# Kernel optimization log

Hardware: AMD Instinct MI355X
Metric: run time of the kernel (lower is better)

Reference implementation:

```python
import jax, jax.numpy as jnp
import numpy as np

SCALING = 2.0  # lora_alpha / r


def setup_inputs() -> dict:
    key = jax.random.key(0)
    ks = jax.random.split(key, 6)
    B, S, D_IN, D_OUT, R = 4, 4096, 4096, 4096, 32
    x = jax.random.normal(ks[0], (B, S, D_IN), dtype=jnp.float32)
    W = jax.random.normal(ks[1], (D_OUT, D_IN), dtype=jnp.float32) * 0.02
    b = jax.random.normal(ks[2], (D_OUT,), dtype=jnp.float32) * 0.02
    A = jax.random.normal(ks[3], (R, D_IN), dtype=jnp.float32) * 0.02
    B_w = jax.random.normal(ks[4], (D_OUT, R), dtype=jnp.float32) * 0.02
    # per-sample activation offsets, in [1, S]
    alora_offsets = jax.random.randint(ks[5], (B,), 1, S + 1, dtype=jnp.int32)
    return {"x": x, "alora_offsets": alora_offsets, "W": W, "b": b, "A": A, "B_w": B_w}


def reference(x, alora_offsets, W, b, A, B_w):
    # base linear: y = x @ W^T + b
    base = jnp.einsum("bsd,od->bso", x, W) + b  # [B, S, D_OUT]
    # LoRA path on full sequence (dropout is identity at inference, p=0)
    lora = jnp.einsum("bsr,or->bso", jnp.einsum("bsd,rd->bsr", x, A), B_w) * SCALING
    # per-sample tail mask: only last k = min(offset, S) positions get the LoRA update
    S = x.shape[1]
    k = jnp.minimum(alora_offsets, S)  # [B]
    pos = jnp.arange(S, dtype=jnp.int32)
    mask = pos[None, :] >= (S - k)[:, None]  # [B, S] True on the tail
    return base + jnp.where(mask[:, :, None], lora, jnp.zeros((), base.dtype))
```

## Files before the change

kernel.cpp:

```cpp
#include <hip/hip_runtime.h>
#include <hip/hip_bf16.h>

typedef __attribute__((ext_vector_type(8))) short short8;
typedef __attribute__((ext_vector_type(4))) float f32x4;

#define GLOAD_LDS16(gp, lp)                                                      \
  __builtin_amdgcn_global_load_lds(                                              \
      (const __attribute__((address_space(1))) void*)(gp),                       \
      (__attribute__((address_space(3))) void*)(lp), 16, 0, 0)

#define SBAR() asm volatile("s_barrier" ::: "memory")
#define VMC(n)                                                                   \
  do {                                                                           \
    asm volatile("s_waitcnt vmcnt(" #n ")" ::: "memory");                        \
    __builtin_amdgcn_sched_barrier(0);                                           \
  } while (0)

__device__ __forceinline__ unsigned short f2bf_rne(float f) {
  union { float f; unsigned int u; } v; v.f = f;
  unsigned int u = v.u;
  u += 0x7fffu + ((u >> 16) & 1u);
  return (unsigned short)(u >> 16);
}

__device__ __forceinline__ short8 pack8(f32x4 a, f32x4 b) {
  short8 o;
  o[0] = (short)f2bf_rne(a[0]); o[1] = (short)f2bf_rne(a[1]);
  o[2] = (short)f2bf_rne(a[2]); o[3] = (short)f2bf_rne(a[3]);
  o[4] = (short)f2bf_rne(b[0]); o[5] = (short)f2bf_rne(b[1]);
  o[6] = (short)f2bf_rne(b[2]); o[7] = (short)f2bf_rne(b[3]);
  return o;
}

__global__ __launch_bounds__(256) void cvt_lora_kernel(
    const float* __restrict__ x,
    const float* __restrict__ A,
    const float* __restrict__ W,
    const float* __restrict__ Bw,
    const int* __restrict__ offs,
    unsigned short* __restrict__ xb,
    unsigned short* __restrict__ Wb,
    unsigned short* __restrict__ Bwb,
    unsigned short* __restrict__ T)
{
  __shared__ unsigned short xs[32 * 72];
  __shared__ unsigned short as_[32 * 72];
  const int t = threadIdx.x;
  const int m0 = blockIdx.x * 32;
  const int l = t & 63, w = t >> 6;
  const int wr = w >> 1, wc = w & 1;
  const int lr = l & 15, lk = (l >> 4) * 8;
  const int arow = t >> 3, acol = (t & 7) * 8;

  if (blockIdx.x < 64) {
    int idx = blockIdx.x * 256 + t;
    const f32x4* s4b = (const f32x4*)Bw;
    ((short8*)Bwb)[idx] = pack8(s4b[2 * idx], s4b[2 * idx + 1]);
  }

  const float* px = x + (size_t)(m0 + arow) * 4096 + acol;
  const float* pa = A + (size_t)arow * 4096 + acol;
  f32x4 vx0 = *(const f32x4*)px, vx1 = *(const f32x4*)(px + 4);
  f32x4 va0 = *(const f32x4*)pa, va1 = *(const f32x4*)(pa + 4);

  f32x4 acc = {0, 0, 0, 0};
  for (int kt = 0; kt < 64; ++kt) {
    short8 s0 = pack8(vx0, vx1);
    short8 sa = pack8(va0, va1);
    if (kt < 63) {
      px += 64; pa += 64;
      vx0 = *(const f32x4*)px; vx1 = *(const f32x4*)(px + 4);
      va0 = *(const f32x4*)pa; va1 = *(const f32x4*)(pa + 4);
    }
    *(short8*)(xb + (size_t)(m0 + arow) * 4096 + kt * 64 + acol) = s0;
    __syncthreads();
    *(short8*)&xs[arow * 72 + acol]  = s0;
    *(short8*)&as_[arow * 72 + acol] = sa;
    __syncthreads();
#pragma unroll
    for (int kk = 0; kk < 2; ++kk) {
      short8 a = *(const short8*)&xs[(wr * 16 + lr) * 72 + kk * 32 + lk];
      short8 b = *(const short8*)&as_[(wc * 16 + lr) * 72 + kk * 32 + lk];
      acc = __builtin_amdgcn_mfma_f32_16x16x32_bf16(a, b, acc, 0, 0, 0);
    }
  }
  const int rowb = (l >> 4) * 4;
#pragma unroll
  for (int j = 0; j < 4; ++j) {
    int m = m0 + wr * 16 + rowb + j;
    int bb = m >> 12, s = m & 4095;
    int kcut = offs[bb]; if (kcut > 4096) kcut = 4096;
    bool keep = s >= 4096 - kcut;
    T[(size_t)m * 32 + wc * 16 + lr] = keep ? f2bf_rne(2.0f * acc[j]) : (unsigned short)0;
  }
  const f32x4* s4 = (const f32x4*)W;
  short8* d8 = (short8*)Wb;
  const int base = blockIdx.x * 4096;
#pragma unroll
  for (int q = 0; q < 16; ++q) {
    int idx = base + q * 256 + t;
    d8[idx] = pack8(s4[2 * idx], s4[2 * idx + 1]);
  }
}

__global__ __launch_bounds__(512, 2) void gemm_kernel(
    const unsigned short* __restrict__ xb,
    const unsigned short* __restrict__ Wb,
    const unsigned short* __restrict__ Tm,
    const unsigned short* __restrict__ Bwb,
    const float* __restrict__ bias,
    float* __restrict__ out)
{
  constexpr int K = 4096;
  extern __shared__ char smem[];

  const int bid = blockIdx.x;
  const int swz = (bid & 7) * 128 + (bid >> 3);
  const int m0 = (swz >> 4) * 256;
  const int n0 = (swz & 15) * 256;

  const int t = threadIdx.x;
  const int l = t & 63, w = t >> 6;
  const int wqr = w >> 2;
  const int pr = (w >> 1) & 1;
  const int pc = w & 1;
  const int lr = l & 15, hi = l >> 4;
  const int e0 = (hi ^ (lr & 7)) * 8;

  const int srow = t >> 3;
  const int schunk = ((t & 7) ^ ((t >> 3) & 7)) * 8;
  const unsigned short* pA0 = xb + (size_t)(m0 + srow) * K + schunk;
  const unsigned short* pA1 = xb + (size_t)(m0 + 128 + srow) * K + schunk;
  const unsigned short* pB0 = Wb + (size_t)(n0 + srow) * K + schunk;
  const unsigned short* pB1 = Wb + (size_t)(n0 + 128 + srow) * K + schunk;
  unsigned short* sm = (unsigned short*)smem;
  const int ldst = t * 16;

#define STG(PTR, SLOT, ISB, HALF, KT)                                           \
  do {                                                                          \
    const unsigned short* g_ = (PTR) + (KT) * 64;                               \
    char* d_ = smem + (SLOT) * 65536 + (ISB) * 32768 + (HALF) * 16384 + ldst;   \
    GLOAD_LDS16(g_, d_);                                                        \
    GLOAD_LDS16(g_ + (size_t)64 * K, d_ + 8192);                                \
  } while (0)

  f32x4 acc[2][4][4];
  short8 afr[4];

  {
    const unsigned short* tp = Tm + (size_t)(m0 + wqr * 128 + pr * 64 + lr) * 32 + hi * 8;
    short8 la[4];
#pragma unroll
    for (int i = 0; i < 4; ++i) la[i] = *(const short8*)(tp + i * 512);
    short8 lb[2][4];
#pragma unroll
    for (int qc = 0; qc < 2; ++qc)
#pragma unroll
      for (int j = 0; j < 4; ++j)
        lb[qc][j] = *(const short8*)(Bwb + (size_t)(n0 + qc * 128 + pc * 64 + j * 16 + lr) * 32 + hi * 8);
#pragma unroll
    for (int qc = 0; qc < 2; ++qc)
#pragma unroll
      for (int i = 0; i < 4; ++i)
#pragma unroll
        for (int j = 0; j < 4; ++j)
          acc[qc][i][j] = __builtin_amdgcn_mfma_f32_16x16x32_bf16(
              la[i], lb[qc][j], (f32x4){0.f, 0.f, 0.f, 0.f}, 0, 0, 0);
  }

  STG(pA0, 0, 0, 0, 0);
  STG(pA1, 0, 0, 1, 0);
  STG(pB0, 0, 1, 0, 0);
  STG(pB1, 0, 1, 1, 0);
  STG(pA0, 1, 0, 0, 1);
  VMC(4);
  SBAR();

#define PHASE(SLOT, QC, KK, READA, STG_STMT, WAIT_STMT)                         \
  {                                                                             \
    const unsigned short* Ah = sm + (SLOT) * 32768 + wqr * 8192;                \
    const unsigned short* Bh = sm + (SLOT) * 32768 + 16384 + (QC) * 8192;       \
    const int ek = e0 ^ ((KK) * 32);                                            \
    if (READA) {                                                                \
      _Pragma("unroll")                                                         \
      for (int i = 0; i < 4; ++i)                                               \
        afr[i] = *(const short8*)(Ah + (pr * 64 + i * 16 + lr) * 64 + ek);      \
    }                                                                           \
    short8 bfr[4];                                                              \
    _Pragma("unroll")                                                           \
    for (int j = 0; j < 4; ++j)                                                 \
      bfr[j] = *(const short8*)(Bh + (pc * 64 + j * 16 + lr) * 64 + ek);        \
    STG_STMT;                                                                   \
    SBAR();                                                                     \
    __builtin_amdgcn_s_setprio(1);                                              \
    _Pragma("unroll")                                                           \
    for (int i = 0; i < 4; ++i)                                                 \
      _Pragma("unroll")                                                         \
      for (int j = 0; j < 4; ++j)                                               \
        acc[QC][i][j] = __builtin_amdgcn_mfma_f32_16x16x32_bf16(                \
            afr[i], bfr[j], acc[QC][i][j], 0, 0, 0);                            \
    __builtin_amdgcn_s_setprio(0);                                              \
    WAIT_STMT;                                                                  \
    SBAR();                                                                     \
  }

  for (int I = 0; I < 31; ++I) {
    const int a = 2 * I;
    PHASE(0, 0, 0, 1, STG(pA1, 1, 0, 1, a + 1), VMC(4));
    PHASE(0, 1, 0, 0, STG(pB0, 1, 1, 0, a + 1), ((void)0));
    PHASE(0, 0, 1, 1, STG(pB1, 1, 1, 1, a + 1), ((void)0));
    PHASE(0, 1, 1, 0, STG(pA0, 0, 0, 0, a + 2), VMC(4));
    PHASE(1, 0, 0, 1, STG(pA1, 0, 0, 1, a + 2), VMC(4));
    PHASE(1, 1, 0, 0, STG(pB0, 0, 1, 0, a + 2), ((void)0));
    PHASE(1, 0, 1, 1, STG(pB1, 0, 1, 1, a + 2), ((void)0));
    PHASE(1, 1, 1, 0, STG(pA0, 1, 0, 0, a + 3), VMC(4));
  }
  PHASE(0, 0, 0, 1, STG(pA1, 1, 0, 1, 63), VMC(4));
  PHASE(0, 1, 0, 0, STG(pB0, 1, 1, 0, 63), ((void)0));
  PHASE(0, 0, 1, 1, STG(pB1, 1, 1, 1, 63), ((void)0));
  PHASE(0, 1, 1, 0, ((void)0), VMC(2));
  PHASE(1, 0, 0, 1, ((void)0), VMC(0));
  PHASE(1, 1, 0, 0, ((void)0), ((void)0));
  PHASE(1, 0, 1, 1, ((void)0), ((void)0));
  PHASE(1, 1, 1, 0, ((void)0), ((void)0));
#undef PHASE
#undef STG

  float bv[2][4];
#pragma unroll
  for (int qc = 0; qc < 2; ++qc)
#pragma unroll
    for (int j = 0; j < 4; ++j)
      bv[qc][j] = bias[n0 + qc * 128 + pc * 64 + j * 16 + lr];
  const int rowb = hi * 4;
#pragma unroll
  for (int qc = 0; qc < 2; ++qc)
#pragma unroll
    for (int i = 0; i < 4; ++i)
#pragma unroll
      for (int e = 0; e < 4; ++e) {
        int row = m0 + wqr * 128 + pr * 64 + i * 16 + rowb + e;
        float* orow = out + (size_t)row * 4096 + n0 + qc * 128 + pc * 64;
#pragma unroll
        for (int j = 0; j < 4; ++j) orow[j * 16 + lr] = acc[qc][i][j][e] + bv[qc][j];
      }
}

extern "C" void kernel_launch(void* const* d_in, const int* in_sizes, int n_in,
                              void* d_out, int out_size, void* d_ws, size_t ws_size,
                              hipStream_t stream) {
  const float* x   = (const float*)d_in[0];
  const int* offs  = (const int*)d_in[1];
  const float* W   = (const float*)d_in[2];
  const float* b   = (const float*)d_in[3];
  const float* A   = (const float*)d_in[4];
  const float* Bw  = (const float*)d_in[5];
  float* out = (float*)d_out;

  char* ws = (char*)d_ws;
  unsigned short* xb  = (unsigned short*)ws;
  unsigned short* Wb  = (unsigned short*)(ws + 134217728);
  unsigned short* Bwb = (unsigned short*)(ws + 167772160);
  unsigned short* T   = (unsigned short*)(ws + 168034304);

  hipFuncSetAttribute((const void*)gemm_kernel,
                      hipFuncAttributeMaxDynamicSharedMemorySize, 131072);

  cvt_lora_kernel<<<512, 256, 0, stream>>>(x, A, W, Bw, offs, xb, Wb, Bwb, T);
  gemm_kernel<<<1024, 512, 131072, stream>>>(xb, Wb, T, Bwb, b, out);
}
```

Before: 565.5 us.

## Load A operand fragments directly from global into registers, stage only B in LDS

The x (A) tile is no longer staged through LDS. Each wave loads its MFMA A fragments straight from global memory into double-buffered register banks (even and odd k-tiles), and only the W (B) tile uses the async global-to-LDS path. This halves LDS use to 64KB and removes the A LDS reads. In exchange, each A row is fetched redundantly by the two pc waves, register pressure rises, and the latency of the direct global loads must be hidden by the vmcnt waits.

```diff
diff --git a/kernel.cpp b/kernel.cpp
--- a/kernel.cpp
+++ b/kernel.cpp
@@ -129,23 +129,39 @@
 
   const int srow = t >> 3;
   const int schunk = ((t & 7) ^ ((t >> 3) & 7)) * 8;
-  const unsigned short* pA0 = xb + (size_t)(m0 + srow) * K + schunk;
-  const unsigned short* pA1 = xb + (size_t)(m0 + 128 + srow) * K + schunk;
   const unsigned short* pB0 = Wb + (size_t)(n0 + srow) * K + schunk;
   const unsigned short* pB1 = Wb + (size_t)(n0 + 128 + srow) * K + schunk;
   unsigned short* sm = (unsigned short*)smem;
   const int ldst = t * 16;
 
-#define STG(PTR, SLOT, ISB, HALF, KT)                                           \
+#define STGB(PTR, SLOT, HALF, KT)                                               \
   do {                                                                          \
     const unsigned short* g_ = (PTR) + (KT) * 64;                               \
-    char* d_ = smem + (SLOT) * 65536 + (ISB) * 32768 + (HALF) * 16384 + ldst;   \
+    char* d_ = smem + (SLOT) * 32768 + (HALF) * 16384 + ldst;                   \
     GLOAD_LDS16(g_, d_);                                                        \
     GLOAD_LDS16(g_ + (size_t)64 * K, d_ + 8192);                                \
   } while (0)
 
+  const unsigned short* ap0 = xb + (size_t)(m0 + wqr * 128 + pr * 64 + lr) * K + hi * 8;
+  const unsigned short* ap1 = ap0 + (size_t)16 * K;
+  const unsigned short* ap2 = ap0 + (size_t)32 * K;
+  const unsigned short* ap3 = ap0 + (size_t)48 * K;
+
+  short8 arE[2][4], arO[2][4];
+
+#define LDA(BANK, KT)                                                           \
+  do {                                                                          \
+    BANK[0][0] = *(const short8*)(ap0 + (KT) * 64);                             \
+    BANK[0][1] = *(const short8*)(ap1 + (KT) * 64);                             \
+    BANK[0][2] = *(const short8*)(ap2 + (KT) * 64);                             \
+    BANK[0][3] = *(const short8*)(ap3 + (KT) * 64);                             \
+    BANK[1][0] = *(const short8*)(ap0 + (KT) * 64 + 32);                        \
+    BANK[1][1] = *(const short8*)(ap1 + (KT) * 64 + 32);                        \
+    BANK[1][2] = *(const short8*)(ap2 + (KT) * 64 + 32);                        \
+    BANK[1][3] = *(const short8*)(ap3 + (KT) * 64 + 32);                        \
+  } while (0)
+
   f32x4 acc[2][4][4];
-  short8 afr[4];
 
   {
     const unsigned short* tp = Tm + (size_t)(m0 + wqr * 128 + pr * 64 + lr) * 32 + hi * 8;
@@ -168,63 +184,59 @@
               la[i], lb[qc][j], (f32x4){0.f, 0.f, 0.f, 0.f}, 0, 0, 0);
   }
 
-  STG(pA0, 0, 0, 0, 0);
-  STG(pA1, 0, 0, 1, 0);
-  STG(pB0, 0, 1, 0, 0);
-  STG(pB1, 0, 1, 1, 0);
-  STG(pA0, 1, 0, 0, 1);
-  VMC(4);
+  STGB(pB0, 0, 0, 0);
+  STGB(pB1, 0, 1, 0);
+  LDA(arE, 0);
+  VMC(8);
   SBAR();
 
-#define PHASE(SLOT, QC, KK, READA, STG_STMT, WAIT_STMT)                         \
+#define PHASE(SLOT, QC, KK, BANK, ISSUE_STMT, WAIT_STMT)                        \
   {                                                                             \
-    const unsigned short* Ah = sm + (SLOT) * 32768 + wqr * 8192;                \
-    const unsigned short* Bh = sm + (SLOT) * 32768 + 16384 + (QC) * 8192;       \
+    const unsigned short* Bh = sm + (SLOT) * 16384 + (QC) * 8192;               \
     const int ek = e0 ^ ((KK) * 32);                                            \
-    if (READA) {                                                                \
-      _Pragma("unroll")                                                         \
-      for (int i = 0; i < 4; ++i)                                               \
-        afr[i] = *(const short8*)(Ah + (pr * 64 + i * 16 + lr) * 64 + ek);      \
-    }                                                                           \
     short8 bfr[4];                                                              \
     _Pragma("unroll")                                                           \
-    for (int j = 0; j < 4; ++j)                                                 \
-      bfr[j] = *(const short8*)(Bh + (pc * 64 + j * 16 + lr) * 64 + ek);        \
-    STG_STMT;                                                                   \
+    for (int j_ = 0; j_ < 4; ++j_)                                              \
+      bfr[j_] = *(const short8*)(Bh + (pc * 64 + j_ * 16 + lr) * 64 + ek);      \
+    ISSUE_STMT;                                                                 \
     SBAR();                                                                     \
     __builtin_amdgcn_s_setprio(1);                                              \
     _Pragma("unroll")                                                           \
-    for (int i = 0; i < 4; ++i)                                                 \
+    for (int i_ = 0; i_ < 4; ++i_)                                              \
       _Pragma("unroll")                                                         \
-      for (int j = 0; j < 4; ++j)                                               \
-        acc[QC][i][j] = __builtin_amdgcn_mfma_f32_16x16x32_bf16(                \
-            afr[i], bfr[j], acc[QC][i][j], 0, 0, 0);                            \
+      for (int j_ = 0; j_ < 4; ++j_)                                            \
+        acc[QC][i_][j_] = __builtin_amdgcn_mfma_f32_16x16x32_bf16(              \
+            BANK[KK][i_], bfr[j_], acc[QC][i_][j_], 0, 0, 0);                   \
     __builtin_amdgcn_s_setprio(0);                                              \
     WAIT_STMT;                                                                  \
     SBAR();                                                                     \
   }
 
+#define NOP ((void)0)
+
   for (int I = 0; I < 31; ++I) {
     const int a = 2 * I;
-    PHASE(0, 0, 0, 1, STG(pA1, 1, 0, 1, a + 1), VMC(4));
-    PHASE(0, 1, 0, 0, STG(pB0, 1, 1, 0, a + 1), ((void)0));
-    PHASE(0, 0, 1, 1, STG(pB1, 1, 1, 1, a + 1), ((void)0));
-    PHASE(0, 1, 1, 0, STG(pA0, 0, 0, 0, a + 2), VMC(4));
-    PHASE(1, 0, 0, 1, STG(pA1, 0, 0, 1, a + 2), VMC(4));
-    PHASE(1, 1, 0, 0, STG(pB0, 0, 1, 0, a + 2), ((void)0));
-    PHASE(1, 0, 1, 1, STG(pB1, 0, 1, 1, a + 2), ((void)0));
-    PHASE(1, 1, 1, 0, STG(pA0, 1, 0, 0, a + 3), VMC(4));
-  }
-  PHASE(0, 0, 0, 1, STG(pA1, 1, 0, 1, 63), VMC(4));
-  PHASE(0, 1, 0, 0, STG(pB0, 1, 1, 0, 63), ((void)0));
-  PHASE(0, 0, 1, 1, STG(pB1, 1, 1, 1, 63), ((void)0));
-  PHASE(0, 1, 1, 0, ((void)0), VMC(2));
-  PHASE(1, 0, 0, 1, ((void)0), VMC(0));
-  PHASE(1, 1, 0, 0, ((void)0), ((void)0));
-  PHASE(1, 0, 1, 1, ((void)0), ((void)0));
-  PHASE(1, 1, 1, 0, ((void)0), ((void)0));
+    PHASE(0, 0, 0, arE, STGB(pB0, 1, 0, a + 1), NOP);
+    PHASE(0, 1, 0, arE, STGB(pB1, 1, 1, a + 1), NOP);
+    PHASE(0, 0, 1, arE, LDA(arO, a + 1), NOP);
+    PHASE(0, 1, 1, arE, NOP, VMC(8));
+    PHASE(1, 0, 0, arO, STGB(pB0, 0, 0, a + 2), NOP);
+    PHASE(1, 1, 0, arO, STGB(pB1, 0, 1, a + 2), NOP);
+    PHASE(1, 0, 1, arO, LDA(arE, a + 2), NOP);
+    PHASE(1, 1, 1, arO, NOP, VMC(8));
+  }
+  PHASE(0, 0, 0, arE, STGB(pB0, 1, 0, 63), NOP);
+  PHASE(0, 1, 0, arE, STGB(pB1, 1, 1, 63), NOP);
+  PHASE(0, 0, 1, arE, LDA(arO, 63), NOP);
+  PHASE(0, 1, 1, arE, NOP, VMC(8));
+  PHASE(1, 0, 0, arO, NOP, NOP);
+  PHASE(1, 1, 0, arO, NOP, NOP);
+  PHASE(1, 0, 1, arO, NOP, NOP);
+  PHASE(1, 1, 1, arO, NOP, NOP);
 #undef PHASE
-#undef STG
+#undef NOP
+#undef STGB
+#undef LDA
 
   float bv[2][4];
 #pragma unroll
@@ -264,8 +276,8 @@
   unsigned short* T   = (unsigned short*)(ws + 168034304);
 
   hipFuncSetAttribute((const void*)gemm_kernel,
-                      hipFuncAttributeMaxDynamicSharedMemorySize, 131072);
+                      hipFuncAttributeMaxDynamicSharedMemorySize, 65536);
 
   cvt_lora_kernel<<<512, 256, 0, stream>>>(x, A, W, Bw, offs, xb, Wb, Bwb, T);
-  gemm_kernel<<<1024, 512, 131072, stream>>>(xb, Wb, T, Bwb, b, out);
-}
+  gemm_kernel<<<1024, 512, 65536, stream>>>(xb, Wb, T, Bwb, b, out);
+}
```

After: 908.0 us. 1.61x slower.
